# Kernel optimization log

Measured on AMD Instinct MI355X. Metric: run time of the kernel, lower is better.

Reference implementation:

```python
import jax, jax.numpy as jnp
import numpy as np
from jax import lax

N, E, T, D = 50000, 400000, 16, 240
HID = 16  # LSTM hidden


def _p(k, shape):
    fan_in = shape[0]
    return jax.random.normal(k, shape, dtype=jnp.float32) * (1.0 / np.sqrt(fan_in))


def setup_inputs() -> dict:
    key = jax.random.key(0)
    ks = jax.random.split(key, 32)
    inp = {
        "x": jax.random.normal(ks[0], (N, D), dtype=jnp.float32),
        "edge_seq": jax.random.normal(ks[1], (E, T, 2), dtype=jnp.float32),
        "node_seq": jax.random.normal(ks[2], (N, T, 2), dtype=jnp.float32),
        # LSTM (torch gate order i,f,g,o); same lstm_edge is used for both edge and node seqs (as in source)
        "lstm_Wih": _p(ks[3], (4 * HID, 2)),
        "lstm_Whh": _p(ks[4], (4 * HID, HID)),
        "lstm_b": jnp.zeros((4 * HID,), jnp.float32),
        "dnn_W": _p(ks[5], (HID, 1)),
        "dnn_b": jnp.zeros((1,), jnp.float32),
        # gat1: in=256, heads=8, out=8 ; gat2: in=64, heads=1, out=64
        "gat1_W": _p(ks[6], (256, 64)),
        "gat1_att": _p(ks[7], (8, 8)),
        "gat1_b": jnp.zeros((64,), jnp.float32),
        "gat2_W": _p(ks[8], (64, 64)),
        "gat2_att": _p(ks[9], (1, 64)),
        "gat2_b": jnp.zeros((64,), jnp.float32),
        "gcn1_W": _p(ks[10], (256, 64)),
        "gcn1_b": jnp.zeros((64,), jnp.float32),
        "gcn2_W": _p(ks[11], (64, 64)),
        "gcn2_b": jnp.zeros((64,), jnp.float32),
        "cls1_W": _p(ks[12], (320, 32)),
        "cls1_b": jnp.zeros((32,), jnp.float32),
        "cls2_W": _p(ks[13], (32, 16)),
        "cls2_b": jnp.zeros((16,), jnp.float32),
        "cls3_W": _p(ks[14], (16, 4)),
        "cls3_b": jnp.zeros((4,), jnp.float32),
        "edge_index": jax.random.randint(ks[15], (2, E), 0, N),
        "edge_len": jax.random.randint(ks[16], (E,), 1, T + 1).astype(jnp.int32),
        "node_len": jax.random.randint(ks[17], (N,), 1, T + 1).astype(jnp.int32),
    }
    return inp


def lstm_last(seq, lens, Wih, Whh, b):
    """Run LSTM over padded [B,T,2] and return hidden at step len-1 (pack/pad_packed semantics)."""
    B, Tt, _ = seq.shape
    H = Whh.shape[1]

    def step(carry, inp):
        h, c, last = carry
        xt, t = inp
        g = xt @ Wih.T + h @ Whh.T + b
        i, f, gg, o = jnp.split(g, 4, axis=-1)
        c = jax.nn.sigmoid(f) * c + jax.nn.sigmoid(i) * jnp.tanh(gg)
        h = jax.nn.sigmoid(o) * jnp.tanh(c)
        last = jnp.where((t == lens - 1)[:, None], h, last)
        return (h, c, last), None

    z = jnp.zeros((B, H), seq.dtype)
    (_, _, last), _ = lax.scan(step, (z, z, z), (jnp.swapaxes(seq, 0, 1), jnp.arange(Tt)))
    return last


def gat_conv(x, src, dst, edge_scalar, W, att, bias, H, C):
    """myGATConv: gather -> leaky_relu -> softmax over dst neighborhoods -> (alpha + edge_mat)*x_j -> scatter-add + residual."""
    n = x.shape[0]
    xh = (x @ W).reshape(n, H, C)                       # [N,H,C]
    alpha = (xh * att[None]).sum(-1)                    # [N,H]
    a = jax.nn.leaky_relu(alpha[src], 0.2)              # [E,H] (alpha_j)
    amax = jax.ops.segment_max(a, dst, num_segments=n)
    ex = jnp.exp(a - amax[dst])
    att_e = ex / jax.ops.segment_sum(ex, dst, num_segments=n)[dst]
    coef = att_e + edge_scalar                          # [E,H] + [E,1] edge bias (edge_mat repeat over heads)
    msg = xh[src] * coef[..., None]                     # [E,H,C]
    out = jax.ops.segment_sum(msg, dst, num_segments=n) + xh  # aggregate + residual
    return out.reshape(n, H * C) + bias


def gcn_conv(x, src, dst, W, b):
    n = x.shape[0]
    xw = x @ W
    deg = jax.ops.segment_sum(jnp.ones(src.shape[0], xw.dtype), dst, num_segments=n) + 1.0  # +self-loop
    dinv = lax.rsqrt(deg)
    norm = (dinv[src] * dinv[dst])[:, None]
    out = jax.ops.segment_sum(xw[src] * norm, dst, num_segments=n) + xw * (dinv * dinv)[:, None]
    return out + b


def reference(x, edge_seq, node_seq, lstm_Wih, lstm_Whh, lstm_b, dnn_W, dnn_b,
              gat1_W, gat1_att, gat1_b, gat2_W, gat2_att, gat2_b,
              gcn1_W, gcn1_b, gcn2_W, gcn2_b,
              cls1_W, cls1_b, cls2_W, cls2_b, cls3_W, cls3_b,
              edge_index, edge_len, node_len):
    src, dst = edge_index[0], edge_index[1]
    # temporal edge branch -> per-edge scalar bias
    edge_feat = lstm_last(edge_seq, edge_len, lstm_Wih, lstm_Whh, lstm_b)   # [E,16]
    edge_scalar = edge_feat @ dnn_W + dnn_b                                 # [E,1]
    # temporal node branch (source reuses lstm_edge) -> concat to node features
    node_feat = lstm_last(node_seq, node_len, lstm_Wih, lstm_Whh, lstm_b)   # [N,16]
    xin = jnp.concatenate([x, node_feat], axis=-1)                          # [N,256]
    # GAT stack (no dropout: eval mode)
    x_gat = gat_conv(xin, src, dst, edge_scalar, gat1_W, gat1_att, gat1_b, 8, 8)
    x_gat = gat_conv(x_gat, src, dst, edge_scalar, gat2_W, gat2_att, gat2_b, 1, 64)
    x_gat = jnp.where(jnp.isinf(x_gat) | jnp.isnan(x_gat), 0.0, x_gat)
    lr = lambda v: jax.nn.leaky_relu(v, 0.01)
    # GCN stack (eval: dropout off)
    x_gcn = lr(gcn_conv(xin, src, dst, gcn1_W, gcn1_b))
    x_gcn = lr(gcn_conv(x_gcn, src, dst, gcn2_W, gcn2_b))
    # classifier head
    h = jnp.concatenate([xin, x_gcn], axis=1)
    h = lr(h @ cls1_W + cls1_b)
    h = lr(h @ cls2_W + cls2_b)
    out = h @ cls3_W + cls3_b
    return (out, x_gcn, x_gat)
```

## Files before the change

kernel.cpp:

```cpp
#include <hip/hip_runtime.h>
#include <hip/hip_bf16.h>


typedef unsigned int u32;

#define NN 50000
#define EE 400000

__device__ float g_nodeF[NN * 16];
__device__ float g_esc[EE];
__device__ float g_P1[NN * 64];
__device__ float g_P2[NN * 64];
__device__ float g_alpha[NN * 8];
__device__ float g_amax[NN * 8];
__device__ float g_rinv[NN * 8];
__device__ float g_dinv[NN];
__device__ int   g_cnt[NN];
__device__ int   g_rs[NN + 1];
__device__ int   g_cur[NN];
__device__ int   g_csrc[EE];
__device__ float g_cesc[EE];
__device__ int   g_bhist[32];
__device__ int   g_bbase[32];
__device__ int   g_permN[NN];
__device__ int   g_permE[EE];
__device__ int   g_bsum[256];
__device__ int   g_boff[256];

__device__ __forceinline__ float rcpf(float x) { return __builtin_amdgcn_rcpf(x); }
__device__ __forceinline__ float sigf(float x) { return rcpf(1.0f + __expf(-x)); }
__device__ __forceinline__ float tanh_fast(float x) {
    return 1.0f - 2.0f * rcpf(__expf(2.0f * x) + 1.0f);
}

typedef short short8 __attribute__((ext_vector_type(8)));
typedef float f32x16 __attribute__((ext_vector_type(16)));

union S8U { short8 v; unsigned u[4]; };

__device__ __forceinline__ unsigned pk_hi(float a, float b) {
    return (__float_as_uint(a) >> 16) | (__float_as_uint(b) & 0xFFFF0000u);
}
__device__ __forceinline__ float bftrunc(float a) {
    return __uint_as_float(__float_as_uint(a) & 0xFFFF0000u);
}
__device__ __forceinline__ float lo_res(float a) { return a - bftrunc(a); }
__device__ __forceinline__ unsigned sx32(unsigned v) {
    return (unsigned)__shfl_xor((int)v, 32, 64);
}

__global__ void __launch_bounds__(256) bucket_hist_kernel(
    const int* __restrict__ nlen, const int* __restrict__ elen)
{
    __shared__ int hb[32];
    int t = threadIdx.x;
    if (t < 32) hb[t] = 0;
    __syncthreads();
    int i = blockIdx.x * 256 + t;
    int bin = -1;
    if (i < NN + EE) {
        bin = (i < NN) ? (16 - nlen[i]) : (32 - elen[i - NN]);
    }
    if (bin >= 0) atomicAdd(&hb[bin], 1);
    __syncthreads();
    if (t < 32 && hb[t] > 0) atomicAdd(&g_bhist[t], hb[t]);
}

__global__ void __launch_bounds__(64) bucket_scan_kernel()
{
    if (threadIdx.x == 0) {
        int acc = 0;
        for (int b = 0; b < 16; ++b) { g_bbase[b] = acc; acc += g_bhist[b]; }
        acc = 0;
        for (int b = 16; b < 32; ++b) { g_bbase[b] = acc; acc += g_bhist[b]; }
    }
}

__global__ void __launch_bounds__(256) bucket_scatter_kernel(
    const int* __restrict__ nlen, const int* __restrict__ elen)
{
    __shared__ int hb[32];
    int t = threadIdx.x;
    if (t < 32) hb[t] = 0;
    __syncthreads();
    int i = blockIdx.x * 256 + t;
    int bin = -1, idx = 0;
    if (i < NN + EE) {
        if (i < NN) { idx = i; bin = 16 - nlen[i]; }
        else        { idx = i - NN; bin = 32 - elen[i - NN]; }
    }
    if (bin >= 0) atomicAdd(&hb[bin], 1);
    __syncthreads();
    if (t < 32) {
        int c = hb[t];
        hb[t] = c > 0 ? atomicAdd(&g_bbase[t], c) : 0;
    }
    __syncthreads();
    if (bin >= 0) {
        int pos = atomicAdd(&hb[bin], 1);
        if (i < NN) g_permN[pos] = idx; else g_permE[pos] = idx;
    }
}

__global__ void __launch_bounds__(256, 3) lstm_fused_kernel(
    const float* __restrict__ nseq, const int* __restrict__ nlen,
    const float* __restrict__ eseq, const int* __restrict__ elen,
    const float* __restrict__ Wih, const float* __restrict__ Whh,
    const float* __restrict__ bias,
    const float* __restrict__ dnnW, const float* __restrict__ dnnb,
    const int* __restrict__ permN, const int* __restrict__ permE,
    float* __restrict__ nodeF, float* __restrict__ esc, int nNodeBlk)
{
    const int lane = threadIdx.x & 63;
    const int col  = lane & 31;
    const int hi   = lane >> 5;
    const bool isLo = (hi == 0);
    const int wave = threadIdx.x >> 6;

    const bool edgeMode = (int)blockIdx.x >= nNodeBlk;
    const float* seq = edgeMode ? eseq : nseq;
    const int*  lens = edgeMode ? elen : nlen;
    const int*  perm = edgeMode ? permE : permN;
    const int limit  = edgeMode ? EE : NN;
    const int bbase  = edgeMode ? ((int)blockIdx.x - nNodeBlk) : (int)blockIdx.x;
    const int g  = bbase * 128 + wave * 32 + col;
    const int gc = g < limit ? g : limit - 1;
    const int s  = perm[gc];
    const bool valid = g < limit;

    const int row0 = col, row1 = col + 32;
    const int ko = hi * 8;
    S8U ahh0, ahh1, ahl0, ahl1, ax0, ax1;
    {
        const float* w0 = Whh + row0 * 16 + ko;
        const float* w1 = Whh + row1 * 16 + ko;
#pragma unroll
        for (int r = 0; r < 4; ++r) {
            float a0 = w0[2 * r], b0 = w0[2 * r + 1];
            float a1 = w1[2 * r], b1 = w1[2 * r + 1];
            ahh0.u[r] = pk_hi(a0, b0);
            ahh1.u[r] = pk_hi(a1, b1);
            ahl0.u[r] = pk_hi(lo_res(a0), lo_res(b0));
            ahl1.u[r] = pk_hi(lo_res(a1), lo_res(b1));
        }
#pragma unroll
        for (int r = 0; r < 4; ++r) { ax0.u[r] = 0u; ax1.u[r] = 0u; }
        if (isLo) {
            float wa0 = Wih[row0 * 2], wb0 = Wih[row0 * 2 + 1], bb0 = bias[row0];
            float wa1 = Wih[row1 * 2], wb1 = Wih[row1 * 2 + 1], bb1 = bias[row1];
            ax0.u[0] = pk_hi(wa0, wb0);
            ax0.u[1] = pk_hi(bb0, wa0);
            ax0.u[2] = pk_hi(wb0, lo_res(wa0));
            ax0.u[3] = pk_hi(lo_res(wb0), lo_res(bb0));
            ax1.u[0] = pk_hi(wa1, wb1);
            ax1.u[1] = pk_hi(bb1, wa1);
            ax1.u[2] = pk_hi(wb1, lo_res(wa1));
            ax1.u[3] = pk_hi(lo_res(wb1), lo_res(bb1));
        }
    }

    const f32x16 zc = {0.f, 0.f, 0.f, 0.f, 0.f, 0.f, 0.f, 0.f,
                       0.f, 0.f, 0.f, 0.f, 0.f, 0.f, 0.f, 0.f};
    const unsigned bxmask = isLo ? 0xFFFFFFFFu : 0u;
    const unsigned one_bf = 0x3F80u;

    float cst[8], hlast[8];
#pragma unroll
    for (int j = 0; j < 8; ++j) { cst[j] = 0.f; hlast[j] = 0.f; }
    unsigned ph[4], pl[4];
#pragma unroll
    for (int r = 0; r < 4; ++r) { ph[r] = 0u; pl[r] = 0u; }

    const float4* sp = (const float4*)seq + (size_t)s * 8;
    const int lenm1 = lens[s] - 1;
    int lm = lenm1;
#pragma unroll
    for (int off = 32; off >= 1; off >>= 1) {
        int o = __shfl_xor(lm, off, 64);
        lm = lm > o ? lm : o;
    }
    const int nIter = (lm >> 1) + 1;

    float4 q = sp[0];
#pragma unroll 1
    for (int i = 0; i < nIter; ++i) {
        float4 qn = sp[(i + 1) & 7];
#pragma unroll
        for (int hf = 0; hf < 2; ++hf) {
            const int t = 2 * i + hf;
            const float x0 = hf ? q.z : q.x;
            const float x1 = hf ? q.w : q.y;

            S8U bhh, bhl, bx;
            {
                unsigned t0 = sx32(ph[0]), t1 = sx32(ph[1]);
                unsigned t2 = sx32(ph[2]), t3 = sx32(ph[3]);
                bhh.u[0] = isLo ? ph[0] : t2;
                bhh.u[1] = isLo ? ph[1] : t3;
                bhh.u[2] = isLo ? t0 : ph[2];
                bhh.u[3] = isLo ? t1 : ph[3];
                unsigned s0 = sx32(pl[0]), s1 = sx32(pl[1]);
                unsigned s2 = sx32(pl[2]), s3 = sx32(pl[3]);
                bhl.u[0] = isLo ? pl[0] : s2;
                bhl.u[1] = isLo ? pl[1] : s3;
                bhl.u[2] = isLo ? s0 : pl[2];
                bhl.u[3] = isLo ? s1 : pl[3];
            }
            {
                float xl0 = lo_res(x0), xl1 = lo_res(x1);
                bx.u[0] = pk_hi(x0, x1) & bxmask;
                bx.u[1] = (one_bf | (__float_as_uint(xl0) & 0xFFFF0000u)) & bxmask;
                bx.u[2] = pk_hi(xl1, x0) & bxmask;
                bx.u[3] = ((__float_as_uint(x1) >> 16) | (one_bf << 16)) & bxmask;
            }

            f32x16 d0 = __builtin_amdgcn_mfma_f32_32x32x16_bf16(ax0.v, bx.v, zc, 0, 0, 0);
            f32x16 d1 = __builtin_amdgcn_mfma_f32_32x32x16_bf16(ax1.v, bx.v, zc, 0, 0, 0);
            d0 = __builtin_amdgcn_mfma_f32_32x32x16_bf16(ahh0.v, bhh.v, d0, 0, 0, 0);
            d1 = __builtin_amdgcn_mfma_f32_32x32x16_bf16(ahh1.v, bhh.v, d1, 0, 0, 0);
            d0 = __builtin_amdgcn_mfma_f32_32x32x16_bf16(ahl0.v, bhh.v, d0, 0, 0, 0);
            d1 = __builtin_amdgcn_mfma_f32_32x32x16_bf16(ahl1.v, bhh.v, d1, 0, 0, 0);
            d0 = __builtin_amdgcn_mfma_f32_32x32x16_bf16(ahh0.v, bhl.v, d0, 0, 0, 0);
            d1 = __builtin_amdgcn_mfma_f32_32x32x16_bf16(ahh1.v, bhl.v, d1, 0, 0, 0);

            float hh[8];
#pragma unroll
            for (int j = 0; j < 8; ++j) {
                float ip = d0[j], fp = d0[8 + j], gp = d1[j], op = d1[8 + j];
                float cu = sigf(fp) * cst[j] + sigf(ip) * tanh_fast(gp);
                cst[j] = cu;
                hh[j] = sigf(op) * tanh_fast(cu);
            }
            const bool selm = (t == lenm1);
#pragma unroll
            for (int j = 0; j < 8; ++j) hlast[j] = selm ? hh[j] : hlast[j];
#pragma unroll
            for (int r = 0; r < 4; ++r) {
                float a = hh[2 * r], b = hh[2 * r + 1];
                ph[r] = pk_hi(a, b);
                pl[r] = pk_hi(lo_res(a), lo_res(b));
            }
        }
        q = qn;
    }

    if (edgeMode) {
        float4 dA = *(const float4*)(dnnW + hi * 4);
        float4 dB = *(const float4*)(dnnW + hi * 4 + 8);
        float part = hlast[0] * dA.x + hlast[1] * dA.y + hlast[2] * dA.z + hlast[3] * dA.w
                   + hlast[4] * dB.x + hlast[5] * dB.y + hlast[6] * dB.z + hlast[7] * dB.w;
        float tot = part + __shfl_xor(part, 32, 64);
        if (isLo && valid) esc[s] = tot + dnnb[0];
    } else {
        if (valid) {
            float* dst = nodeF + (size_t)s * 16 + hi * 4;
            *(float4*)(dst)     = make_float4(hlast[0], hlast[1], hlast[2], hlast[3]);
            *(float4*)(dst + 8) = make_float4(hlast[4], hlast[5], hlast[6], hlast[7]);
        }
    }
}

__global__ void __launch_bounds__(256) zero_cnt_kernel(int* cnt, int n)
{
    int t = blockIdx.x * 256 + threadIdx.x;
    if (t < n) cnt[t] = 0;
    if (blockIdx.x == 0 && threadIdx.x < 32) g_bhist[threadIdx.x] = 0;
}
__global__ void __launch_bounds__(256) count_kernel(const int* __restrict__ dst,
                                                    int* cnt, int E)
{
    int e = blockIdx.x * 256 + threadIdx.x;
    if (e < E) atomicAdd(&cnt[dst[e]], 1);
}

__global__ void __launch_bounds__(256) scan1_kernel(const int* __restrict__ cnt, int n)
{
    __shared__ int s[256];
    int t = threadIdx.x;
    int i = blockIdx.x * 256 + t;
    s[t] = (i < n) ? cnt[i] : 0;
    __syncthreads();
#pragma unroll
    for (int off = 128; off >= 1; off >>= 1) {
        if (t < off) s[t] += s[t + off];
        __syncthreads();
    }
    if (t == 0) g_bsum[blockIdx.x] = s[0];
}

__global__ void __launch_bounds__(256) scan2_kernel(int nb)
{
    __shared__ int s[256];
    int t = threadIdx.x;
    int v = (t < nb) ? g_bsum[t] : 0;
    s[t] = v;
    __syncthreads();
#pragma unroll
    for (int off = 1; off < 256; off <<= 1) {
        int add = (t >= off) ? s[t - off] : 0;
        __syncthreads();
        s[t] += add;
        __syncthreads();
    }
    if (t < nb) g_boff[t] = s[t] - v;
}

__global__ void __launch_bounds__(256) scan3_kernel(
    const int* __restrict__ cnt, int* __restrict__ rs, int* __restrict__ cur,
    float* __restrict__ dinv, int n, int E)
{
    __shared__ int s[256];
    int t = threadIdx.x;
    int i = blockIdx.x * 256 + t;
    int v = (i < n) ? cnt[i] : 0;
    s[t] = v;
    __syncthreads();
#pragma unroll
    for (int off = 1; off < 256; off <<= 1) {
        int add = (t >= off) ? s[t - off] : 0;
        __syncthreads();
        s[t] += add;
        __syncthreads();
    }
    if (i < n) {
        int excl = s[t] - v + g_boff[blockIdx.x];
        rs[i] = excl;
        cur[i] = excl;
        dinv[i] = rsqrtf((float)v + 1.0f);
    }
    if (i == 0) rs[n] = E;
}

__global__ void __launch_bounds__(256) fill_kernel(const int* __restrict__ src,
                                                   const int* __restrict__ dst,
                                                   const float* __restrict__ esc,
                                                   int* __restrict__ cur,
                                                   int* __restrict__ csrc,
                                                   float* __restrict__ cesc, int E)
{
    int e = blockIdx.x * 256 + threadIdx.x;
    if (e >= E) return;
    int pos = atomicAdd(&cur[dst[e]], 1);
    csrc[pos] = src[e];
    cesc[pos] = esc[e];
}

__global__ void __launch_bounds__(256, 2) gemmX_mfma_kernel(
    const float* __restrict__ x, const float* __restrict__ nodeF,
    const float* __restrict__ W, float* __restrict__ C, int n)
{
    __shared__ unsigned sWhi[128 * 64];
    __shared__ unsigned sWlo[128 * 64];
    const int tid = threadIdx.x;
    for (int i = tid; i < 128 * 64; i += 256) {
        const int kk2 = i >> 6, c = i & 63;
        float a = W[kk2 * 128 + c];
        float b = W[kk2 * 128 + 64 + c];
        sWhi[i] = pk_hi(a, b);
        sWlo[i] = pk_hi(lo_res(a), lo_res(b));
    }
    __syncthreads();

    const int lane = tid & 63;
    const int col  = lane & 31;
    const int hi   = lane >> 5;
    const int wv   = tid >> 6;
    const int nodeBase = blockIdx.x * 128 + wv * 32;
    const int nodeL = nodeBase + col;
    const int nc = nodeL < n ? nodeL : n - 1;

    const f32x16 zc = {0.f, 0.f, 0.f, 0.f, 0.f, 0.f, 0.f, 0.f,
                       0.f, 0.f, 0.f, 0.f, 0.f, 0.f, 0.f, 0.f};
    f32x16 acc0 = zc, acc1 = zc;
    const float* xrow = x + (size_t)nc * 240;
    const float* frow = nodeF + (size_t)nc * 16;

#pragma unroll 1
    for (int ch = 0; ch < 16; ++ch) {
        const float* src = (ch < 15) ? (xrow + ch * 16 + hi * 8) : (frow + hi * 8);
        float4 v0 = *(const float4*)src;
        float4 v1 = *(const float4*)(src + 4);
        S8U xh, xl;
        xh.u[0] = pk_hi(v0.x, v0.y);
        xh.u[1] = pk_hi(v0.z, v0.w);
        xh.u[2] = pk_hi(v1.x, v1.y);
        xh.u[3] = pk_hi(v1.z, v1.w);
        xl.u[0] = pk_hi(lo_res(v0.x), lo_res(v0.y));
        xl.u[1] = pk_hi(lo_res(v0.z), lo_res(v0.w));
        xl.u[2] = pk_hi(lo_res(v1.x), lo_res(v1.y));
        xl.u[3] = pk_hi(lo_res(v1.z), lo_res(v1.w));

        const int rbase = (ch * 8 + hi * 4) * 64 + col;
        S8U wh0, wl0, wh1, wl1;
#pragma unroll
        for (int r = 0; r < 4; ++r) {
            wh0.u[r] = sWhi[rbase + r * 64];
            wl0.u[r] = sWlo[rbase + r * 64];
            wh1.u[r] = sWhi[rbase + r * 64 + 32];
            wl1.u[r] = sWlo[rbase + r * 64 + 32];
        }
        acc0 = __builtin_amdgcn_mfma_f32_32x32x16_bf16(xh.v, wh0.v, acc0, 0, 0, 0);
        acc1 = __builtin_amdgcn_mfma_f32_32x32x16_bf16(xh.v, wh1.v, acc1, 0, 0, 0);
        acc0 = __builtin_amdgcn_mfma_f32_32x32x16_bf16(xl.v, wh0.v, acc0, 0, 0, 0);
        acc1 = __builtin_amdgcn_mfma_f32_32x32x16_bf16(xl.v, wh1.v, acc1, 0, 0, 0);
        acc0 = __builtin_amdgcn_mfma_f32_32x32x16_bf16(xh.v, wl0.v, acc0, 0, 0, 0);
        acc1 = __builtin_amdgcn_mfma_f32_32x32x16_bf16(xh.v, wl1.v, acc1, 0, 0, 0);
    }

#pragma unroll
    for (int r = 0; r < 16; ++r) {
        const int nr = (r & 3) + 8 * (r >> 2) + 4 * hi;
        const int nd = nodeBase + nr;
        if (nd < n) {
            C[(size_t)nd * 64 + col]      = acc0[r];
            C[(size_t)nd * 64 + 32 + col] = acc1[r];
        }
    }
}

__global__ void __launch_bounds__(256, 2) gemm64_mfma_kernel(
    const float* __restrict__ A, const float* __restrict__ W,
    float* __restrict__ C, int n)
{
    __shared__ unsigned sWhi[32 * 64];
    __shared__ unsigned sWlo[32 * 64];
    const int tid = threadIdx.x;
    for (int i = tid; i < 32 * 64; i += 256) {
        const int kk2 = i >> 6, c = i & 63;
        float a = W[kk2 * 128 + c];
        float b = W[kk2 * 128 + 64 + c];
        sWhi[i] = pk_hi(a, b);
        sWlo[i] = pk_hi(lo_res(a), lo_res(b));
    }
    __syncthreads();

    const int lane = tid & 63;
    const int col  = lane & 31;
    const int hi   = lane >> 5;
    const int wv   = tid >> 6;
    const int nodeBase = blockIdx.x * 128 + wv * 32;
    const int nodeL = nodeBase + col;
    const int nc = nodeL < n ? nodeL : n - 1;

    const f32x16 zc = {0.f, 0.f, 0.f, 0.f, 0.f, 0.f, 0.f, 0.f,
                       0.f, 0.f, 0.f, 0.f, 0.f, 0.f, 0.f, 0.f};
    f32x16 acc0 = zc, acc1 = zc;
    const float* arow = A + (size_t)nc * 64;

#pragma unroll
    for (int ch = 0; ch < 4; ++ch) {
        const float* src = arow + ch * 16 + hi * 8;
        float4 v0 = *(const float4*)src;
        float4 v1 = *(const float4*)(src + 4);
        S8U xh, xl;
        xh.u[0] = pk_hi(v0.x, v0.y);
        xh.u[1] = pk_hi(v0.z, v0.w);
        xh.u[2] = pk_hi(v1.x, v1.y);
        xh.u[3] = pk_hi(v1.z, v1.w);
        xl.u[0] = pk_hi(lo_res(v0.x), lo_res(v0.y));
        xl.u[1] = pk_hi(lo_res(v0.z), lo_res(v0.w));
        xl.u[2] = pk_hi(lo_res(v1.x), lo_res(v1.y));
        xl.u[3] = pk_hi(lo_res(v1.z), lo_res(v1.w));

        const int rbase = (ch * 8 + hi * 4) * 64 + col;
        S8U wh0, wl0, wh1, wl1;
#pragma unroll
        for (int r = 0; r < 4; ++r) {
            wh0.u[r] = sWhi[rbase + r * 64];
            wl0.u[r] = sWlo[rbase + r * 64];
            wh1.u[r] = sWhi[rbase + r * 64 + 32];
            wl1.u[r] = sWlo[rbase + r * 64 + 32];
        }
        acc0 = __builtin_amdgcn_mfma_f32_32x32x16_bf16(xh.v, wh0.v, acc0, 0, 0, 0);
        acc1 = __builtin_amdgcn_mfma_f32_32x32x16_bf16(xh.v, wh1.v, acc1, 0, 0, 0);
        acc0 = __builtin_amdgcn_mfma_f32_32x32x16_bf16(xl.v, wh0.v, acc0, 0, 0, 0);
        acc1 = __builtin_amdgcn_mfma_f32_32x32x16_bf16(xl.v, wh1.v, acc1, 0, 0, 0);
        acc0 = __builtin_amdgcn_mfma_f32_32x32x16_bf16(xh.v, wl0.v, acc0, 0, 0, 0);
        acc1 = __builtin_amdgcn_mfma_f32_32x32x16_bf16(xh.v, wl1.v, acc1, 0, 0, 0);
    }

#pragma unroll
    for (int r = 0; r < 16; ++r) {
        const int nr = (r & 3) + 8 * (r >> 2) + 4 * hi;
        const int nd = nodeBase + nr;
        if (nd < n) {
            C[(size_t)nd * 64 + col]      = acc0[r];
            C[(size_t)nd * 64 + 32 + col] = acc1[r];
        }
    }
}

template <int H, int C>
__global__ void __launch_bounds__(256) alpha_kernel(const float* __restrict__ xh,
                                                    const float* __restrict__ att,
                                                    float* __restrict__ alpha, int n)
{
    int t = blockIdx.x * 256 + threadIdx.x;
    if (t >= n * H) return;
    int h = (H == 1) ? 0 : (t % H);
    int nd = (H == 1) ? t : (t / H);
    const float* row = xh + (size_t)nd * 64 + h * C;
    float s = 0.f;
#pragma unroll
    for (int c = 0; c < C; ++c) s += row[c] * att[h * C + c];
    alpha[t] = s;
}

__global__ void __launch_bounds__(256) gat_softmax8_row_kernel(
    const int* __restrict__ rs, const int* __restrict__ csrc,
    const float* __restrict__ alpha,
    float* __restrict__ amax, float* __restrict__ rinv, int n)
{
    int d = blockIdx.x * 256 + threadIdx.x;
    if (d >= n) return;
    int k0 = rs[d], k1 = rs[d + 1];
    float m[8];
#pragma unroll
    for (int h = 0; h < 8; ++h) m[h] = -INFINITY;
    for (int k = k0; k < k1; ++k) {
        const float4* ar = (const float4*)(alpha + (size_t)csrc[k] * 8);
        float4 a0 = ar[0], a1 = ar[1];
        float v[8] = {a0.x, a0.y, a0.z, a0.w, a1.x, a1.y, a1.z, a1.w};
#pragma unroll
        for (int h = 0; h < 8; ++h) {
            float a = v[h] > 0.f ? v[h] : 0.2f * v[h];
            m[h] = fmaxf(m[h], a);
        }
    }
    float sm[8];
#pragma unroll
    for (int h = 0; h < 8; ++h) sm[h] = 0.f;
    for (int k = k0; k < k1; ++k) {
        const float4* ar = (const float4*)(alpha + (size_t)csrc[k] * 8);
        float4 a0 = ar[0], a1 = ar[1];
        float v[8] = {a0.x, a0.y, a0.z, a0.w, a1.x, a1.y, a1.z, a1.w};
#pragma unroll
        for (int h = 0; h < 8; ++h) {
            float a = v[h] > 0.f ? v[h] : 0.2f * v[h];
            sm[h] += __expf(a - m[h]);
        }
    }
    float4* mo = (float4*)(amax + (size_t)d * 8);
    mo[0] = make_float4(m[0], m[1], m[2], m[3]);
    mo[1] = make_float4(m[4], m[5], m[6], m[7]);
    float4* ro = (float4*)(rinv + (size_t)d * 8);
    ro[0] = make_float4(rcpf(sm[0]), rcpf(sm[1]), rcpf(sm[2]), rcpf(sm[3]));
    ro[1] = make_float4(rcpf(sm[4]), rcpf(sm[5]), rcpf(sm[6]), rcpf(sm[7]));
}

template <int H>
__global__ void __launch_bounds__(256) gat_softmax_csr_kernel(
    const int* __restrict__ rs, const int* __restrict__ csrc,
    const float* __restrict__ alpha,
    float* __restrict__ amax, float* __restrict__ rinv, int n)
{
    int t = blockIdx.x * 256 + threadIdx.x;
    if (t >= n * H) return;
    int h = (H == 1) ? 0 : (t % H);
    int d = (H == 1) ? t : (t / H);
    int k0 = rs[d], k1 = rs[d + 1];
    float m = -INFINITY;
    for (int k = k0; k < k1; ++k) {
        float a = alpha[(size_t)csrc[k] * H + h];
        a = a > 0.f ? a : 0.2f * a;
        m = fmaxf(m, a);
    }
    float s = 0.f;
    for (int k = k0; k < k1; ++k) {
        float a = alpha[(size_t)csrc[k] * H + h];
        a = a > 0.f ? a : 0.2f * a;
        s += __expf(a - m);
    }
    amax[t] = m;
    rinv[t] = rcpf(s);
}

template <int H, bool FILTER>
__global__ void __launch_bounds__(256) gat_gather_kernel(
    const int* __restrict__ rs, const int* __restrict__ csrc,
    const float* __restrict__ cesc,
    const float* __restrict__ xh, const float* __restrict__ alpha,
    const float* __restrict__ amax, const float* __restrict__ rinv,
    const float* __restrict__ bias, float* __restrict__ out, int n)
{
    int j = threadIdx.x & 63;
    int d = blockIdx.x * 4 + (threadIdx.x >> 6);
    if (d >= n) return;
    int h = (H == 8) ? (j >> 3) : 0;
    float m = amax[(size_t)d * H + h];
    float ri = rinv[(size_t)d * H + h];
    float acc = xh[(size_t)d * 64 + j] + bias[j];
    int k1 = rs[d + 1];
#pragma unroll 2
    for (int k = rs[d]; k < k1; ++k) {
        int s = csrc[k];
        float a = alpha[(size_t)s * H + h];
        a = a > 0.f ? a : 0.2f * a;
        float coef = __expf(a - m) * ri + cesc[k];
        acc += xh[(size_t)s * 64 + j] * coef;
    }
    if (FILTER && !__builtin_isfinite(acc)) acc = 0.f;
    out[(size_t)d * 64 + j] = acc;
}

__global__ void __launch_bounds__(256) gcn_gather_kernel(
    const int* __restrict__ rs, const int* __restrict__ csrc,
    const float* __restrict__ xw, const float* __restrict__ dinv,
    const float* __restrict__ bias, float* __restrict__ out, int n)
{
    int j = threadIdx.x & 63;
    int d = blockIdx.x * 4 + (threadIdx.x >> 6);
    if (d >= n) return;
    float di = dinv[d];
    float acc = xw[(size_t)d * 64 + j] * di * di + bias[j];
    int k1 = rs[d + 1];
#pragma unroll 2
    for (int k = rs[d]; k < k1; ++k) {
        int s = csrc[k];
        acc += xw[(size_t)s * 64 + j] * (dinv[s] * di);
    }
    out[(size_t)d * 64 + j] = acc > 0.f ? acc : 0.01f * acc;
}

__global__ void __launch_bounds__(256) cls_kernel(
    const float* __restrict__ x, const float* __restrict__ nodeF,
    const float* __restrict__ xg,
    const float* __restrict__ W1, const float* __restrict__ b1,
    const float* __restrict__ W2, const float* __restrict__ b2,
    const float* __restrict__ W3, const float* __restrict__ b3,
    float* __restrict__ outp, int n)
{
    __shared__ float sW1[320 * 32];
    __shared__ float sW2[32 * 16];
    __shared__ float sW3[16 * 4];
    __shared__ float sb1[32], sb2[16], sb3[4];
    int tid = threadIdx.x;
    for (int i = tid; i < 320 * 32; i += 256) sW1[i] = W1[i];
    for (int i = tid; i < 512; i += 256) sW2[i] = W2[i];
    if (tid < 64) sW3[tid] = W3[tid];
    if (tid < 32) sb1[tid] = b1[tid];
    if (tid < 16) sb2[tid] = b2[tid];
    if (tid < 4)  sb3[tid] = b3[tid];
    __syncthreads();
    int nd = blockIdx.x * 256 + tid;
    if (nd >= n) return;

    float a1[32];
#pragma unroll
    for (int j = 0; j < 32; ++j) a1[j] = sb1[j];
    const float4* xr = (const float4*)(x + (size_t)nd * 240);
#pragma unroll 1
    for (int k4 = 0; k4 < 60; ++k4) {
        float4 v = xr[k4];
        const float* wr = sW1 + k4 * 128;
#pragma unroll
        for (int j = 0; j < 32; ++j)
            a1[j] += v.x * wr[j] + v.y * wr[32 + j] + v.z * wr[64 + j] + v.w * wr[96 + j];
    }
    const float4* nf = (const float4*)(nodeF + (size_t)nd * 16);
#pragma unroll 1
    for (int k4 = 60; k4 < 64; ++k4) {
        float4 v = nf[k4 - 60];
        const float* wr = sW1 + k4 * 128;
#pragma unroll
        for (int j = 0; j < 32; ++j)
            a1[j] += v.x * wr[j] + v.y * wr[32 + j] + v.z * wr[64 + j] + v.w * wr[96 + j];
    }
    const float4* p2 = (const float4*)(xg + (size_t)nd * 64);
#pragma unroll 1
    for (int k4 = 0; k4 < 16; ++k4) {
        float4 v = p2[k4];
        const float* wr = sW1 + 8192 + k4 * 128;
#pragma unroll
        for (int j = 0; j < 32; ++j)
            a1[j] += v.x * wr[j] + v.y * wr[32 + j] + v.z * wr[64 + j] + v.w * wr[96 + j];
    }
#pragma unroll
    for (int j = 0; j < 32; ++j) { float v = a1[j]; a1[j] = v > 0.f ? v : 0.01f * v; }

    float a2[16];
#pragma unroll
    for (int j = 0; j < 16; ++j) a2[j] = sb2[j];
#pragma unroll
    for (int k = 0; k < 32; ++k) {
        float v = a1[k];
        const float* wr = sW2 + k * 16;
#pragma unroll
        for (int j = 0; j < 16; ++j) a2[j] += v * wr[j];
    }
#pragma unroll
    for (int j = 0; j < 16; ++j) { float v = a2[j]; a2[j] = v > 0.f ? v : 0.01f * v; }

    float a3[4] = {sb3[0], sb3[1], sb3[2], sb3[3]};
#pragma unroll
    for (int k = 0; k < 16; ++k) {
        float v = a2[k];
        const float* wr = sW3 + k * 4;
        a3[0] += v * wr[0]; a3[1] += v * wr[1]; a3[2] += v * wr[2]; a3[3] += v * wr[3];
    }
    float4 o = make_float4(a3[0], a3[1], a3[2], a3[3]);
    *(float4*)(outp + (size_t)nd * 4) = o;
}

static inline unsigned nblk(size_t t) { return (unsigned)((t + 255) / 256); }

extern "C" void kernel_launch(void* const* d_in, const int* in_sizes, int n_in,
                              void* d_out, int out_size, void* d_ws, size_t ws_size,
                              hipStream_t stream)
{
    const float* x     = (const float*)d_in[0];
    const float* eseq  = (const float*)d_in[1];
    const float* nseq  = (const float*)d_in[2];
    const float* Wih   = (const float*)d_in[3];
    const float* Whh   = (const float*)d_in[4];
    const float* lb    = (const float*)d_in[5];
    const float* dnnW  = (const float*)d_in[6];
    const float* dnnb  = (const float*)d_in[7];
    const float* g1W   = (const float*)d_in[8];
    const float* g1att = (const float*)d_in[9];
    const float* g1b   = (const float*)d_in[10];
    const float* g2W   = (const float*)d_in[11];
    const float* g2att = (const float*)d_in[12];
    const float* g2b   = (const float*)d_in[13];
    const float* gc1W  = (const float*)d_in[14];
    const float* gc1b  = (const float*)d_in[15];
    const float* gc2W  = (const float*)d_in[16];
    const float* gc2b  = (const float*)d_in[17];
    const float* c1W   = (const float*)d_in[18];
    const float* c1b   = (const float*)d_in[19];
    const float* c2W   = (const float*)d_in[20];
    const float* c2b   = (const float*)d_in[21];
    const float* c3W   = (const float*)d_in[22];
    const float* c3b   = (const float*)d_in[23];
    const int* eidx  = (const int*)d_in[24];
    const int* elen  = (const int*)d_in[25];
    const int* nlen  = (const int*)d_in[26];

    const int N = NN;
    const int E = EE;
    const int* srcp = eidx;
    const int* dstp = eidx + E;

    float *nodeF, *esc, *P1, *P2, *alpha, *amax, *rinv, *dinv, *cesc;
    int *cnt, *rs, *cur, *csrc, *permN, *permE;
    hipGetSymbolAddress((void**)&nodeF, HIP_SYMBOL(g_nodeF));
    hipGetSymbolAddress((void**)&esc,   HIP_SYMBOL(g_esc));
    hipGetSymbolAddress((void**)&P1,    HIP_SYMBOL(g_P1));
    hipGetSymbolAddress((void**)&P2,    HIP_SYMBOL(g_P2));
    hipGetSymbolAddress((void**)&alpha, HIP_SYMBOL(g_alpha));
    hipGetSymbolAddress((void**)&amax,  HIP_SYMBOL(g_amax));
    hipGetSymbolAddress((void**)&rinv,  HIP_SYMBOL(g_rinv));
    hipGetSymbolAddress((void**)&dinv,  HIP_SYMBOL(g_dinv));
    hipGetSymbolAddress((void**)&cnt,   HIP_SYMBOL(g_cnt));
    hipGetSymbolAddress((void**)&rs,    HIP_SYMBOL(g_rs));
    hipGetSymbolAddress((void**)&cur,   HIP_SYMBOL(g_cur));
    hipGetSymbolAddress((void**)&csrc,  HIP_SYMBOL(g_csrc));
    hipGetSymbolAddress((void**)&cesc,  HIP_SYMBOL(g_cesc));
    hipGetSymbolAddress((void**)&permN, HIP_SYMBOL(g_permN));
    hipGetSymbolAddress((void**)&permE, HIP_SYMBOL(g_permE));

    float* out0   = (float*)d_out;
    float* outGcn = out0 + (size_t)N * 4;
    float* outGat = outGcn + (size_t)N * 64;

    zero_cnt_kernel<<<nblk(N), 256, 0, stream>>>(cnt, N);
    bucket_hist_kernel<<<nblk(NN + EE), 256, 0, stream>>>(nlen, elen);
    bucket_scan_kernel<<<1, 64, 0, stream>>>();
    bucket_scatter_kernel<<<nblk(NN + EE), 256, 0, stream>>>(nlen, elen);

    const int nNodeBlk = (N + 127) / 128;
    const int nEdgeBlk = (E + 127) / 128;
    lstm_fused_kernel<<<nNodeBlk + nEdgeBlk, 256, 0, stream>>>(
        nseq, nlen, eseq, elen, Wih, Whh, lb, dnnW, dnnb, permN, permE,
        nodeF, esc, nNodeBlk);

    const unsigned scanBlk = nblk(N);
    count_kernel<<<nblk(E), 256, 0, stream>>>(dstp, cnt, E);
    scan1_kernel<<<scanBlk, 256, 0, stream>>>(cnt, N);
    scan2_kernel<<<1, 256, 0, stream>>>((int)scanBlk);
    scan3_kernel<<<scanBlk, 256, 0, stream>>>(cnt, rs, cur, dinv, N, E);
    fill_kernel<<<nblk(E), 256, 0, stream>>>(srcp, dstp, esc, cur, csrc, cesc, E);

    const unsigned gemmBlk = (N + 127) / 128;

    gemmX_mfma_kernel<<<gemmBlk, 256, 0, stream>>>(x, nodeF, g1W, P1, N);
    alpha_kernel<8, 8><<<nblk((size_t)N * 8), 256, 0, stream>>>(P1, g1att, alpha, N);
    gat_softmax8_row_kernel<<<nblk(N), 256, 0, stream>>>(rs, csrc, alpha, amax, rinv, N);
    gat_gather_kernel<8, false><<<(N + 3) / 4, 256, 0, stream>>>(
        rs, csrc, cesc, P1, alpha, amax, rinv, g1b, P2, N);

    gemm64_mfma_kernel<<<gemmBlk, 256, 0, stream>>>(P2, g2W, P1, N);
    alpha_kernel<1, 64><<<nblk(N), 256, 0, stream>>>(P1, g2att, alpha, N);
    gat_softmax_csr_kernel<1><<<nblk(N), 256, 0, stream>>>(rs, csrc, alpha, amax, rinv, N);
    gat_gather_kernel<1, true><<<(N + 3) / 4, 256, 0, stream>>>(
        rs, csrc, cesc, P1, alpha, amax, rinv, g2b, outGat, N);

    gemmX_mfma_kernel<<<gemmBlk, 256, 0, stream>>>(x, nodeF, gc1W, P1, N);
    gcn_gather_kernel<<<(N + 3) / 4, 256, 0, stream>>>(rs, csrc, P1, dinv, gc1b, P2, N);

    gemm64_mfma_kernel<<<gemmBlk, 256, 0, stream>>>(P2, gc2W, P1, N);
    gcn_gather_kernel<<<(N + 3) / 4, 256, 0, stream>>>(rs, csrc, P1, dinv, gc2b, outGcn, N);

    cls_kernel<<<nblk(N), 256, 0, stream>>>(x, nodeF, outGcn, c1W, c1b, c2W, c2b, c3W, c3b, out0, N);
}
```

Before: 628.9 us.

## Fuse GAT softmax into gather and merge GAT/GCN gathers per layer

Computes the GAT per-destination softmax max and sum inside the gather kernel with an online softmax and wave shuffles, removing the separate softmax kernels and the amax/rinv buffers. It also runs the GAT and GCN aggregations in one kernel per layer so both walk the CSR edge list once, and folds the degree count into the histogram kernel and the block-offset scan into scan3. This cuts kernel launches and repeated csrc/alpha traversals, at the cost of two extra 64-wide buffers and more registers per thread in the combined gather.

```diff
diff --git a/kernel.cpp b/kernel.cpp
--- a/kernel.cpp
+++ b/kernel.cpp
@@ -11,9 +11,9 @@
 __device__ float g_esc[EE];
 __device__ float g_P1[NN * 64];
 __device__ float g_P2[NN * 64];
+__device__ float g_P3[NN * 64];
+__device__ float g_P4[NN * 64];
 __device__ float g_alpha[NN * 8];
-__device__ float g_amax[NN * 8];
-__device__ float g_rinv[NN * 8];
 __device__ float g_dinv[NN];
 __device__ int   g_cnt[NN];
 __device__ int   g_rs[NN + 1];
@@ -25,7 +25,6 @@
 __device__ int   g_permN[NN];
 __device__ int   g_permE[EE];
 __device__ int   g_bsum[256];
-__device__ int   g_boff[256];
 
 __device__ __forceinline__ float rcpf(float x) { return __builtin_amdgcn_rcpf(x); }
 __device__ __forceinline__ float sigf(float x) { return rcpf(1.0f + __expf(-x)); }
@@ -50,7 +49,8 @@
 }
 
 __global__ void __launch_bounds__(256) bucket_hist_kernel(
-    const int* __restrict__ nlen, const int* __restrict__ elen)
+    const int* __restrict__ nlen, const int* __restrict__ elen,
+    const int* __restrict__ dstp, int* __restrict__ cnt)
 {
     __shared__ int hb[32];
     int t = threadIdx.x;
@@ -62,6 +62,7 @@
         bin = (i < NN) ? (16 - nlen[i]) : (32 - elen[i - NN]);
     }
     if (bin >= 0) atomicAdd(&hb[bin], 1);
+    if (i < EE) atomicAdd(&cnt[dstp[i]], 1);
     __syncthreads();
     if (t < 32 && hb[t] > 0) atomicAdd(&g_bhist[t], hb[t]);
 }
@@ -266,12 +267,6 @@
     if (t < n) cnt[t] = 0;
     if (blockIdx.x == 0 && threadIdx.x < 32) g_bhist[threadIdx.x] = 0;
 }
-__global__ void __launch_bounds__(256) count_kernel(const int* __restrict__ dst,
-                                                    int* cnt, int E)
-{
-    int e = blockIdx.x * 256 + threadIdx.x;
-    if (e < E) atomicAdd(&cnt[dst[e]], 1);
-}
 
 __global__ void __launch_bounds__(256) scan1_kernel(const int* __restrict__ cnt, int n)
 {
@@ -288,11 +283,26 @@
     if (t == 0) g_bsum[blockIdx.x] = s[0];
 }
 
-__global__ void __launch_bounds__(256) scan2_kernel(int nb)
-{
+__global__ void __launch_bounds__(256) scan3_kernel(
+    const int* __restrict__ cnt, int* __restrict__ rs, int* __restrict__ cur,
+    float* __restrict__ dinv, int n, int E, int nb)
+{
+    __shared__ int sb[256];
     __shared__ int s[256];
     int t = threadIdx.x;
-    int v = (t < nb) ? g_bsum[t] : 0;
+    sb[t] = (t < nb) ? g_bsum[t] : 0;
+    __syncthreads();
+#pragma unroll
+    for (int off = 1; off < 256; off <<= 1) {
+        int add = (t >= off) ? sb[t - off] : 0;
+        __syncthreads();
+        sb[t] += add;
+        __syncthreads();
+    }
+    const int boff = (blockIdx.x == 0) ? 0 : sb[blockIdx.x - 1];
+
+    int i = blockIdx.x * 256 + t;
+    int v = (i < n) ? cnt[i] : 0;
     s[t] = v;
     __syncthreads();
 #pragma unroll
@@ -302,28 +312,8 @@
         s[t] += add;
         __syncthreads();
     }
-    if (t < nb) g_boff[t] = s[t] - v;
-}
-
-__global__ void __launch_bounds__(256) scan3_kernel(
-    const int* __restrict__ cnt, int* __restrict__ rs, int* __restrict__ cur,
-    float* __restrict__ dinv, int n, int E)
-{
-    __shared__ int s[256];
-    int t = threadIdx.x;
-    int i = blockIdx.x * 256 + t;
-    int v = (i < n) ? cnt[i] : 0;
-    s[t] = v;
-    __syncthreads();
-#pragma unroll
-    for (int off = 1; off < 256; off <<= 1) {
-        int add = (t >= off) ? s[t - off] : 0;
-        __syncthreads();
-        s[t] += add;
-        __syncthreads();
-    }
     if (i < n) {
-        int excl = s[t] - v + g_boff[blockIdx.x];
+        int excl = s[t] - v + boff;
         rs[i] = excl;
         cur[i] = excl;
         dinv[i] = rsqrtf((float)v + 1.0f);
@@ -506,120 +496,92 @@
     alpha[t] = s;
 }
 
-__global__ void __launch_bounds__(256) gat_softmax8_row_kernel(
+template <int H, bool FILTER>
+__global__ void __launch_bounds__(256) fused_gather_kernel(
     const int* __restrict__ rs, const int* __restrict__ csrc,
-    const float* __restrict__ alpha,
-    float* __restrict__ amax, float* __restrict__ rinv, int n)
-{
-    int d = blockIdx.x * 256 + threadIdx.x;
+    const float* __restrict__ cesc, const float* __restrict__ alpha,
+    const float* __restrict__ xh, const float* __restrict__ xw,
+    const float* __restrict__ dinv,
+    const float* __restrict__ gbias, const float* __restrict__ cbias,
+    float* __restrict__ gout, float* __restrict__ cout, int n)
+{
+    const int j = threadIdx.x & 63;
+    const int d = blockIdx.x * 4 + (threadIdx.x >> 6);
     if (d >= n) return;
-    int k0 = rs[d], k1 = rs[d + 1];
-    float m[8];
-#pragma unroll
-    for (int h = 0; h < 8; ++h) m[h] = -INFINITY;
+    const int k0 = rs[d], k1 = rs[d + 1];
+
+    float m = -INFINITY, ssum = 0.f;
+    if (H == 8) {
+        const int e = j >> 3, h = j & 7;
+        const int nb = (k1 - k0 + 7) >> 3;
+        for (int b = 0; b < nb; ++b) {
+            int k = k0 + b * 8 + e;
+            if (k < k1) {
+                float a = alpha[(size_t)csrc[k] * 8 + h];
+                a = a > 0.f ? a : 0.2f * a;
+                float mn = fmaxf(m, a);
+                ssum = ssum * __expf(m - mn) + __expf(a - mn);
+                m = mn;
+            }
+        }
+#pragma unroll
+        for (int msk = 8; msk <= 32; msk <<= 1) {
+            float mo = __shfl_xor(m, msk, 64);
+            float so = __shfl_xor(ssum, msk, 64);
+            float mn = fmaxf(m, mo);
+            float f1 = (m == -INFINITY) ? 0.f : __expf(m - mn);
+            float f2 = (mo == -INFINITY) ? 0.f : __expf(mo - mn);
+            ssum = ssum * f1 + so * f2;
+            m = mn;
+        }
+    } else {
+        const int nb = (k1 - k0 + 63) >> 6;
+        for (int b = 0; b < nb; ++b) {
+            int k = k0 + b * 64 + j;
+            if (k < k1) {
+                float a = alpha[csrc[k]];
+                a = a > 0.f ? a : 0.2f * a;
+                float mn = fmaxf(m, a);
+                ssum = ssum * __expf(m - mn) + __expf(a - mn);
+                m = mn;
+            }
+        }
+#pragma unroll
+        for (int msk = 1; msk <= 32; msk <<= 1) {
+            float mo = __shfl_xor(m, msk, 64);
+            float so = __shfl_xor(ssum, msk, 64);
+            float mn = fmaxf(m, mo);
+            float f1 = (m == -INFINITY) ? 0.f : __expf(m - mn);
+            float f2 = (mo == -INFINITY) ? 0.f : __expf(mo - mn);
+            ssum = ssum * f1 + so * f2;
+            m = mn;
+        }
+    }
+    const int h2 = (H == 8) ? (j >> 3) : 0;
+    float mh, ri;
+    if (H == 8) {
+        mh = __shfl(m, h2, 64);
+        ri = rcpf(__shfl(ssum, h2, 64));
+    } else {
+        mh = m;
+        ri = rcpf(ssum);
+    }
+
+    const float di = dinv[d];
+    float ag = xh[(size_t)d * 64 + j] + gbias[j];
+    float ac = xw[(size_t)d * 64 + j] * di * di + cbias[j];
+#pragma unroll 2
     for (int k = k0; k < k1; ++k) {
-        const float4* ar = (const float4*)(alpha + (size_t)csrc[k] * 8);
-        float4 a0 = ar[0], a1 = ar[1];
-        float v[8] = {a0.x, a0.y, a0.z, a0.w, a1.x, a1.y, a1.z, a1.w};
-#pragma unroll
-        for (int h = 0; h < 8; ++h) {
-            float a = v[h] > 0.f ? v[h] : 0.2f * v[h];
-            m[h] = fmaxf(m[h], a);
-        }
-    }
-    float sm[8];
-#pragma unroll
-    for (int h = 0; h < 8; ++h) sm[h] = 0.f;
-    for (int k = k0; k < k1; ++k) {
-        const float4* ar = (const float4*)(alpha + (size_t)csrc[k] * 8);
-        float4 a0 = ar[0], a1 = ar[1];
-        float v[8] = {a0.x, a0.y, a0.z, a0.w, a1.x, a1.y, a1.z, a1.w};
-#pragma unroll
-        for (int h = 0; h < 8; ++h) {
-            float a = v[h] > 0.f ? v[h] : 0.2f * v[h];
-            sm[h] += __expf(a - m[h]);
-        }
-    }
-    float4* mo = (float4*)(amax + (size_t)d * 8);
-    mo[0] = make_float4(m[0], m[1], m[2], m[3]);
-    mo[1] = make_float4(m[4], m[5], m[6], m[7]);
-    float4* ro = (float4*)(rinv + (size_t)d * 8);
-    ro[0] = make_float4(rcpf(sm[0]), rcpf(sm[1]), rcpf(sm[2]), rcpf(sm[3]));
-    ro[1] = make_float4(rcpf(sm[4]), rcpf(sm[5]), rcpf(sm[6]), rcpf(sm[7]));
-}
-
-template <int H>
-__global__ void __launch_bounds__(256) gat_softmax_csr_kernel(
-    const int* __restrict__ rs, const int* __restrict__ csrc,
-    const float* __restrict__ alpha,
-    float* __restrict__ amax, float* __restrict__ rinv, int n)
-{
-    int t = blockIdx.x * 256 + threadIdx.x;
-    if (t >= n * H) return;
-    int h = (H == 1) ? 0 : (t % H);
-    int d = (H == 1) ? t : (t / H);
-    int k0 = rs[d], k1 = rs[d + 1];
-    float m = -INFINITY;
-    for (int k = k0; k < k1; ++k) {
-        float a = alpha[(size_t)csrc[k] * H + h];
+        int s = csrc[k];
+        float a = alpha[(size_t)s * H + h2];
         a = a > 0.f ? a : 0.2f * a;
-        m = fmaxf(m, a);
-    }
-    float s = 0.f;
-    for (int k = k0; k < k1; ++k) {
-        float a = alpha[(size_t)csrc[k] * H + h];
-        a = a > 0.f ? a : 0.2f * a;
-        s += __expf(a - m);
-    }
-    amax[t] = m;
-    rinv[t] = rcpf(s);
-}
-
-template <int H, bool FILTER>
-__global__ void __launch_bounds__(256) gat_gather_kernel(
-    const int* __restrict__ rs, const int* __restrict__ csrc,
-    const float* __restrict__ cesc,
-    const float* __restrict__ xh, const float* __restrict__ alpha,
-    const float* __restrict__ amax, const float* __restrict__ rinv,
-    const float* __restrict__ bias, float* __restrict__ out, int n)
-{
-    int j = threadIdx.x & 63;
-    int d = blockIdx.x * 4 + (threadIdx.x >> 6);
-    if (d >= n) return;
-    int h = (H == 8) ? (j >> 3) : 0;
-    float m = amax[(size_t)d * H + h];
-    float ri = rinv[(size_t)d * H + h];
-    float acc = xh[(size_t)d * 64 + j] + bias[j];
-    int k1 = rs[d + 1];
-#pragma unroll 2
-    for (int k = rs[d]; k < k1; ++k) {
-        int s = csrc[k];
-        float a = alpha[(size_t)s * H + h];
-        a = a > 0.f ? a : 0.2f * a;
-        float coef = __expf(a - m) * ri + cesc[k];
-        acc += xh[(size_t)s * 64 + j] * coef;
-    }
-    if (FILTER && !__builtin_isfinite(acc)) acc = 0.f;
-    out[(size_t)d * 64 + j] = acc;
-}
-
-__global__ void __launch_bounds__(256) gcn_gather_kernel(
-    const int* __restrict__ rs, const int* __restrict__ csrc,
-    const float* __restrict__ xw, const float* __restrict__ dinv,
-    const float* __restrict__ bias, float* __restrict__ out, int n)
-{
-    int j = threadIdx.x & 63;
-    int d = blockIdx.x * 4 + (threadIdx.x >> 6);
-    if (d >= n) return;
-    float di = dinv[d];
-    float acc = xw[(size_t)d * 64 + j] * di * di + bias[j];
-    int k1 = rs[d + 1];
-#pragma unroll 2
-    for (int k = rs[d]; k < k1; ++k) {
-        int s = csrc[k];
-        acc += xw[(size_t)s * 64 + j] * (dinv[s] * di);
-    }
-    out[(size_t)d * 64 + j] = acc > 0.f ? acc : 0.01f * acc;
+        float coef = __expf(a - mh) * ri + cesc[k];
+        ag += xh[(size_t)s * 64 + j] * coef;
+        ac += xw[(size_t)s * 64 + j] * (dinv[s] * di);
+    }
+    if (FILTER && !__builtin_isfinite(ag)) ag = 0.f;
+    gout[(size_t)d * 64 + j] = ag;
+    cout[(size_t)d * 64 + j] = ac > 0.f ? ac : 0.01f * ac;
 }
 
 __global__ void __launch_bounds__(256) cls_kernel(
@@ -741,15 +703,15 @@
     const int* srcp = eidx;
     const int* dstp = eidx + E;
 
-    float *nodeF, *esc, *P1, *P2, *alpha, *amax, *rinv, *dinv, *cesc;
+    float *nodeF, *esc, *P1, *P2, *P3, *P4, *alpha, *dinv, *cesc;
     int *cnt, *rs, *cur, *csrc, *permN, *permE;
     hipGetSymbolAddress((void**)&nodeF, HIP_SYMBOL(g_nodeF));
     hipGetSymbolAddress((void**)&esc,   HIP_SYMBOL(g_esc));
     hipGetSymbolAddress((void**)&P1,    HIP_SYMBOL(g_P1));
     hipGetSymbolAddress((void**)&P2,    HIP_SYMBOL(g_P2));
+    hipGetSymbolAddress((void**)&P3,    HIP_SYMBOL(g_P3));
+    hipGetSymbolAddress((void**)&P4,    HIP_SYMBOL(g_P4));
     hipGetSymbolAddress((void**)&alpha, HIP_SYMBOL(g_alpha));
-    hipGetSymbolAddress((void**)&amax,  HIP_SYMBOL(g_amax));
-    hipGetSymbolAddress((void**)&rinv,  HIP_SYMBOL(g_rinv));
     hipGetSymbolAddress((void**)&dinv,  HIP_SYMBOL(g_dinv));
     hipGetSymbolAddress((void**)&cnt,   HIP_SYMBOL(g_cnt));
     hipGetSymbolAddress((void**)&rs,    HIP_SYMBOL(g_rs));
@@ -764,7 +726,7 @@
     float* outGat = outGcn + (size_t)N * 64;
 
     zero_cnt_kernel<<<nblk(N), 256, 0, stream>>>(cnt, N);
-    bucket_hist_kernel<<<nblk(NN + EE), 256, 0, stream>>>(nlen, elen);
+    bucket_hist_kernel<<<nblk(NN + EE), 256, 0, stream>>>(nlen, elen, dstp, cnt);
     bucket_scan_kernel<<<1, 64, 0, stream>>>();
     bucket_scatter_kernel<<<nblk(NN + EE), 256, 0, stream>>>(nlen, elen);
 
@@ -775,31 +737,23 @@
         nodeF, esc, nNodeBlk);
 
     const unsigned scanBlk = nblk(N);
-    count_kernel<<<nblk(E), 256, 0, stream>>>(dstp, cnt, E);
     scan1_kernel<<<scanBlk, 256, 0, stream>>>(cnt, N);
-    scan2_kernel<<<1, 256, 0, stream>>>((int)scanBlk);
-    scan3_kernel<<<scanBlk, 256, 0, stream>>>(cnt, rs, cur, dinv, N, E);
+    scan3_kernel<<<scanBlk, 256, 0, stream>>>(cnt, rs, cur, dinv, N, E, (int)scanBlk);
     fill_kernel<<<nblk(E), 256, 0, stream>>>(srcp, dstp, esc, cur, csrc, cesc, E);
 
     const unsigned gemmBlk = (N + 127) / 128;
 
     gemmX_mfma_kernel<<<gemmBlk, 256, 0, stream>>>(x, nodeF, g1W, P1, N);
+    gemmX_mfma_kernel<<<gemmBlk, 256, 0, stream>>>(x, nodeF, gc1W, P3, N);
     alpha_kernel<8, 8><<<nblk((size_t)N * 8), 256, 0, stream>>>(P1, g1att, alpha, N);
-    gat_softmax8_row_kernel<<<nblk(N), 256, 0, stream>>>(rs, csrc, alpha, amax, rinv, N);
-    gat_gather_kernel<8, false><<<(N + 3) / 4, 256, 0, stream>>>(
-        rs, csrc, cesc, P1, alpha, amax, rinv, g1b, P2, N);
+    fused_gather_kernel<8, false><<<(N + 3) / 4, 256, 0, stream>>>(
+        rs, csrc, cesc, alpha, P1, P3, dinv, g1b, gc1b, P2, P4, N);
 
     gemm64_mfma_kernel<<<gemmBlk, 256, 0, stream>>>(P2, g2W, P1, N);
+    gemm64_mfma_kernel<<<gemmBlk, 256, 0, stream>>>(P4, gc2W, P3, N);
     alpha_kernel<1, 64><<<nblk(N), 256, 0, stream>>>(P1, g2att, alpha, N);
-    gat_softmax_csr_kernel<1><<<nblk(N), 256, 0, stream>>>(rs, csrc, alpha, amax, rinv, N);
-    gat_gather_kernel<1, true><<<(N + 3) / 4, 256, 0, stream>>>(
-        rs, csrc, cesc, P1, alpha, amax, rinv, g2b, outGat, N);
-
-    gemmX_mfma_kernel<<<gemmBlk, 256, 0, stream>>>(x, nodeF, gc1W, P1, N);
-    gcn_gather_kernel<<<(N + 3) / 4, 256, 0, stream>>>(rs, csrc, P1, dinv, gc1b, P2, N);
-
-    gemm64_mfma_kernel<<<gemmBlk, 256, 0, stream>>>(P2, gc2W, P1, N);
-    gcn_gather_kernel<<<(N + 3) / 4, 256, 0, stream>>>(rs, csrc, P1, dinv, gc2b, outGcn, N);
+    fused_gather_kernel<1, true><<<(N + 3) / 4, 256, 0, stream>>>(
+        rs, csrc, cesc, alpha, P1, P3, dinv, g2b, gc2b, outGat, outGcn, N);
 
     cls_kernel<<<nblk(N), 256, 0, stream>>>(x, nodeF, outGcn, c1W, c1b, c2W, c2b, c3W, c3b, out0, N);
 }
```

New measurement: 560.9 us. 10.8% less time.
